# Kernel optimization log

Hardware: AMD Instinct MI355X
Metric: run time of the kernel (lower is better)

## Reference

```python
import jax, jax.numpy as jnp
import numpy as np

NUM_WIRES = 4
N_LAYERS = 2
HIDDEN = 64
NUM_CLASSES = 10
B = 4096


def _ry(state, theta, wire):
    # state: (N,2,2,2,2); theta: scalar or (N,)
    st = jnp.moveaxis(state, wire + 1, 1)
    c = jnp.reshape(jnp.cos(theta / 2), (-1, 1, 1, 1))
    s = jnp.reshape(jnp.sin(theta / 2), (-1, 1, 1, 1))
    n0 = c * st[:, 0] - s * st[:, 1]
    n1 = s * st[:, 0] + c * st[:, 1]
    st = jnp.stack([n0, n1], axis=1)
    return jnp.moveaxis(st, 1, wire + 1)


def _cnot(state, ctrl, tgt):
    st = jnp.moveaxis(state, (ctrl + 1, tgt + 1), (1, 2))  # (N,2,2,2,2)
    st = jnp.stack([st[:, 0], st[:, 1, ::-1]], axis=1)
    return jnp.moveaxis(st, (1, 2), (ctrl + 1, tgt + 1))


def _zexp(state, wire):
    p = state * state  # real statevector -> probabilities
    axes = tuple(a for a in range(1, 5) if a != wire + 1)
    marg = p.sum(axes)  # (N,2)
    return marg[:, 0] - marg[:, 1]


def quantum_layer(angles, vparams):
    # angles: (N,4) data rotation angles; vparams: (2,4)
    N = angles.shape[0]
    state = jnp.zeros((N, 2, 2, 2, 2), angles.dtype).at[:, 0, 0, 0, 0].set(1.0)
    for w in range(NUM_WIRES):
        state = _ry(state, angles[:, w], w)
    for l in range(N_LAYERS):
        for w in range(NUM_WIRES):
            state = _ry(state, vparams[l, w], w)
        state = _cnot(state, 0, 1)
        state = _cnot(state, 1, 2)
        state = _cnot(state, 2, 3)
    return jnp.stack([_zexp(state, w) for w in range(NUM_WIRES)], axis=1)  # (N,4)


def setup_inputs() -> dict:
    key = jax.random.key(0)
    ks = jax.random.split(key, 8)
    x = jax.random.uniform(ks[0], (B, 28, 28), dtype=jnp.float32)
    vparams = jax.random.normal(ks[1], (N_LAYERS, NUM_WIRES), dtype=jnp.float32)
    w1 = jax.random.normal(ks[2], (HIDDEN, NUM_WIRES), dtype=jnp.float32) * 0.5
    b1 = jnp.zeros((HIDDEN,), jnp.float32)
    w2 = jax.random.normal(ks[3], (1, HIDDEN), dtype=jnp.float32) * 0.125
    b2 = jnp.zeros((1,), jnp.float32)
    W = jax.random.normal(ks[4], (NUM_CLASSES, NUM_WIRES * 14 * 14), dtype=jnp.float32) * 0.03
    b = jnp.zeros((NUM_CLASSES,), jnp.float32)
    return {"x": x, "vparams": vparams, "w1": w1, "b1": b1, "w2": w2, "b2": b2, "W": W, "b": b}


def reference(x, vparams, w1, b1, w2, b2, W, b):
    Bx = x.shape[0]
    # 2x2 stride-2 patches, order [(r,c),(r,c+1),(r+1,c),(r+1,c+1)], patches row-major
    patches = x.reshape(Bx, 14, 2, 14, 2).transpose(0, 1, 3, 2, 4).reshape(Bx, 196, 4)
    meas = quantum_layer(patches.reshape(-1, 4), vparams).reshape(Bx, 196, 4)
    h = jax.nn.relu(jnp.einsum('bpn,hn->bph', meas, w1) + b1)
    scores = (jnp.einsum('bph,oh->bpo', h, w2) + b2)[..., 0]  # (B,196)
    attn = jax.nn.softmax(scores, axis=1)[..., None]
    weighted = meas * attn
    flat = weighted.reshape(Bx, -1)  # (B,784)
    logits = flat @ W.T + b
    return jax.nn.log_softmax(logits, axis=-1)
```

## Files before the change

kernel.cpp:

```cpp
#include <hip/hip_runtime.h>
#include <math.h>

#define NP 196
#define NC 10

template<int CTRL>
__device__ __forceinline__ float dpp_sum_step(float x) {
    int t = __builtin_amdgcn_update_dpp(0, __float_as_int(x), CTRL, 0xf, 0xf, false);
    return x + __int_as_float(t);
}
template<int CTRL>
__device__ __forceinline__ float dpp_max_step(float x) {
    int xi = __float_as_int(x);
    int t = __builtin_amdgcn_update_dpp(xi, xi, CTRL, 0xf, 0xf, false);
    return fmaxf(x, __int_as_float(t));
}
__device__ __forceinline__ float wave_sum(float x) {
    x = dpp_sum_step<0x111>(x);
    x = dpp_sum_step<0x112>(x);
    x = dpp_sum_step<0x114>(x);
    x = dpp_sum_step<0x118>(x);
    x = dpp_sum_step<0x142>(x);
    x = dpp_sum_step<0x143>(x);
    return __int_as_float(__builtin_amdgcn_readlane(__float_as_int(x), 63));
}
__device__ __forceinline__ float wave_max(float x) {
    x = dpp_max_step<0x111>(x);
    x = dpp_max_step<0x112>(x);
    x = dpp_max_step<0x114>(x);
    x = dpp_max_step<0x118>(x);
    x = dpp_max_step<0x142>(x);
    x = dpp_max_step<0x143>(x);
    return __int_as_float(__builtin_amdgcn_readlane(__float_as_int(x), 63));
}

__global__ __launch_bounds__(256) void quanv_fused(
    const float* __restrict__ x,
    const float* __restrict__ vparams,
    const float* __restrict__ w1,
    const float* __restrict__ b1,
    const float* __restrict__ w2,
    const float* __restrict__ b2,
    const float* __restrict__ W,
    const float* __restrict__ bias,
    float* __restrict__ out)
{
    __shared__ float s_red_max[4];
    __shared__ float s_red_sum[4];
    __shared__ float s_lred[4][NC];
    __shared__ float s_logits[NC];

    const int tid  = threadIdx.x;
    const int b    = blockIdx.x;
    const int lane = tid & 63;
    const int wv   = tid >> 6;

    float meas0 = 0.f, meas1 = 0.f, meas2 = 0.f, meas3 = 0.f;
    float myscore = -INFINITY;
    if (tid < NP) {
        const int pr = tid / 14;
        const int pc = tid - pr * 14;
        const float* px = x + (size_t)b * 784 + (2 * pr) * 28 + 2 * pc;
        const float2 ra = *(const float2*)px;
        const float2 rb = *(const float2*)(px + 28);

        float cw[4], sw[4];
        __sincosf((ra.x + vparams[0]) * 0.5f, &sw[0], &cw[0]);
        __sincosf((ra.y + vparams[1]) * 0.5f, &sw[1], &cw[1]);
        __sincosf((rb.x + vparams[2]) * 0.5f, &sw[2], &cw[2]);
        __sincosf((rb.y + vparams[3]) * 0.5f, &sw[3], &cw[3]);

        float t[4] = {cw[0]*cw[1], cw[0]*sw[1], sw[0]*cw[1], sw[0]*sw[1]};
        float u[4] = {cw[2]*cw[3], cw[2]*sw[3], sw[2]*cw[3], sw[2]*sw[3]};
        float v[16];
        #pragma unroll
        for (int i = 0; i < 16; i++) v[i] = t[i >> 2] * u[i & 3];

        #pragma unroll
        for (int i = 0; i < 16; i++)
            if ((i & 8) && !(i & 4)) { const float tm = v[i]; v[i] = v[i | 4]; v[i | 4] = tm; }
        #pragma unroll
        for (int i = 0; i < 16; i++)
            if ((i & 4) && !(i & 2)) { const float tm = v[i]; v[i] = v[i | 2]; v[i | 2] = tm; }
        #pragma unroll
        for (int i = 0; i < 16; i++)
            if ((i & 2) && !(i & 1)) { const float tm = v[i]; v[i] = v[i | 1]; v[i | 1] = tm; }

        #pragma unroll
        for (int w = 0; w < 4; w++) {
            float c, s;
            __sincosf(vparams[4 + w] * 0.5f, &s, &c);
            const int m = 8 >> w;
            #pragma unroll
            for (int i = 0; i < 16; i++) {
                if ((i & m) == 0) {
                    const float v0 = v[i], v1 = v[i | m];
                    v[i]     = c * v0 - s * v1;
                    v[i | m] = s * v0 + c * v1;
                }
            }
        }
        #pragma unroll
        for (int i = 0; i < 16; i++)
            if ((i & 8) && !(i & 4)) { const float tm = v[i]; v[i] = v[i | 4]; v[i | 4] = tm; }
        #pragma unroll
        for (int i = 0; i < 16; i++)
            if ((i & 4) && !(i & 2)) { const float tm = v[i]; v[i] = v[i | 2]; v[i | 2] = tm; }
        #pragma unroll
        for (int i = 0; i < 16; i++)
            if ((i & 2) && !(i & 1)) { const float tm = v[i]; v[i] = v[i | 1]; v[i | 1] = tm; }

        float p[16];
        #pragma unroll
        for (int i = 0; i < 16; i++) p[i] = v[i] * v[i];
        float e[8], d[8];
        #pragma unroll
        for (int j = 0; j < 8; j++) { e[j] = p[2*j] + p[2*j+1]; d[j] = p[2*j] - p[2*j+1]; }
        meas3 = ((d[0]+d[1]) + (d[2]+d[3])) + ((d[4]+d[5]) + (d[6]+d[7]));
        float f[4], g[4];
        #pragma unroll
        for (int k = 0; k < 4; k++) { f[k] = e[2*k] + e[2*k+1]; g[k] = e[2*k] - e[2*k+1]; }
        meas2 = (g[0]+g[1]) + (g[2]+g[3]);
        meas1 = (f[0]-f[1]) + (f[2]-f[3]);
        meas0 = (f[0]+f[1]) - (f[2]+f[3]);

        float sc = b2[0];
        #pragma unroll
        for (int j = 0; j < 64; j++) {
            float h = fmaf(w1[j * 4 + 0], meas0, fmaf(w1[j * 4 + 1], meas1,
                      fmaf(w1[j * 4 + 2], meas2, fmaf(w1[j * 4 + 3], meas3, b1[j]))));
            h = fmaxf(h, 0.f);
            sc = fmaf(w2[j], h, sc);
        }
        myscore = sc;
    }

    float mx = wave_max(myscore);
    if (lane == 0) s_red_max[wv] = mx;
    __syncthreads();
    const float gmax = fmaxf(fmaxf(s_red_max[0], s_red_max[1]),
                             fmaxf(s_red_max[2], s_red_max[3]));
    const float e2 = (tid < NP) ? __expf(myscore - gmax) : 0.f;
    float sm = wave_sum(e2);
    if (lane == 0) s_red_sum[wv] = sm;
    __syncthreads();
    const float gsum = s_red_sum[0] + s_red_sum[1] + s_red_sum[2] + s_red_sum[3];
    const float attn = e2 / gsum;

    float acc[NC];
    #pragma unroll
    for (int o = 0; o < NC; o++) acc[o] = 0.f;
    if (tid < NP) {
        const float wm0 = attn * meas0, wm1 = attn * meas1;
        const float wm2 = attn * meas2, wm3 = attn * meas3;
        #pragma unroll
        for (int o = 0; o < NC; o++) {
            const float4 Wv = *(const float4*)(W + o * 784 + tid * 4);
            acc[o] = fmaf(wm0, Wv.x, fmaf(wm1, Wv.y, fmaf(wm2, Wv.z, wm3 * Wv.w)));
        }
    }
    #pragma unroll
    for (int o = 0; o < NC; o++) {
        const float a = wave_sum(acc[o]);
        if (lane == 0) s_lred[wv][o] = a;
    }
    __syncthreads();
    if (tid < NC) {
        s_logits[tid] = bias[tid] + s_lred[0][tid] + s_lred[1][tid]
                      + s_lred[2][tid] + s_lred[3][tid];
    }
    __syncthreads();
    if (tid < NC) {
        float lmax = s_logits[0];
        #pragma unroll
        for (int i = 1; i < NC; i++) lmax = fmaxf(lmax, s_logits[i]);
        float lse = 0.f;
        #pragma unroll
        for (int i = 0; i < NC; i++) lse += __expf(s_logits[i] - lmax);
        out[(size_t)b * NC + tid] = s_logits[tid] - lmax - __logf(lse);
    }
}

extern "C" void kernel_launch(void* const* d_in, const int* in_sizes, int n_in,
                              void* d_out, int out_size, void* d_ws, size_t ws_size,
                              hipStream_t stream) {
    const float* x       = (const float*)d_in[0];
    const float* vparams = (const float*)d_in[1];
    const float* w1      = (const float*)d_in[2];
    const float* b1      = (const float*)d_in[3];
    const float* w2      = (const float*)d_in[4];
    const float* b2      = (const float*)d_in[5];
    const float* W       = (const float*)d_in[6];
    const float* bias    = (const float*)d_in[7];
    float* out           = (float*)d_out;

    const int B = in_sizes[0] / 784;
    quanv_fused<<<B, 256, 0, stream>>>(x, vparams, w1, b1, w2, b2, W, bias, out);
}
```

Before: 94.83 us.

## Drop softmax max pass and merge normalizer into single reduction round

Removes the max-subtraction pass of the attention softmax, computing exp(score) directly and folding the normalizing sum into the same reduction as the ten logit partial sums. Reductions now use 16-lane DPP row sums written to shared memory and summed by 11 threads, cutting a block barrier and the cross-row DPP steps. Out-of-range threads are clamped to a valid patch so the per-patch math runs without branching, and the hidden-layer loop uses two accumulators. Skipping the max subtraction risks overflow or precision loss if scores become large.

Result: faster. 90.13 us (-5.0%).

```diff
diff --git a/kernel.cpp b/kernel.cpp
--- a/kernel.cpp
+++ b/kernel.cpp
@@ -9,29 +9,12 @@
     int t = __builtin_amdgcn_update_dpp(0, __float_as_int(x), CTRL, 0xf, 0xf, false);
     return x + __int_as_float(t);
 }
-template<int CTRL>
-__device__ __forceinline__ float dpp_max_step(float x) {
-    int xi = __float_as_int(x);
-    int t = __builtin_amdgcn_update_dpp(xi, xi, CTRL, 0xf, 0xf, false);
-    return fmaxf(x, __int_as_float(t));
-}
-__device__ __forceinline__ float wave_sum(float x) {
+__device__ __forceinline__ float row16_sum(float x) {
     x = dpp_sum_step<0x111>(x);
     x = dpp_sum_step<0x112>(x);
     x = dpp_sum_step<0x114>(x);
     x = dpp_sum_step<0x118>(x);
-    x = dpp_sum_step<0x142>(x);
-    x = dpp_sum_step<0x143>(x);
-    return __int_as_float(__builtin_amdgcn_readlane(__float_as_int(x), 63));
-}
-__device__ __forceinline__ float wave_max(float x) {
-    x = dpp_max_step<0x111>(x);
-    x = dpp_max_step<0x112>(x);
-    x = dpp_max_step<0x114>(x);
-    x = dpp_max_step<0x118>(x);
-    x = dpp_max_step<0x142>(x);
-    x = dpp_max_step<0x143>(x);
-    return __int_as_float(__builtin_amdgcn_readlane(__float_as_int(x), 63));
+    return x;
 }
 
 __global__ __launch_bounds__(256) void quanv_fused(
@@ -45,131 +28,128 @@
     const float* __restrict__ bias,
     float* __restrict__ out)
 {
-    __shared__ float s_red_max[4];
-    __shared__ float s_red_sum[4];
-    __shared__ float s_lred[4][NC];
+    __shared__ float s_part[11][16];
+    __shared__ float s_tot[11];
     __shared__ float s_logits[NC];
 
     const int tid  = threadIdx.x;
     const int b    = blockIdx.x;
     const int lane = tid & 63;
     const int wv   = tid >> 6;
+    const int pt   = (tid < NP) ? tid : NP - 1;
 
-    float meas0 = 0.f, meas1 = 0.f, meas2 = 0.f, meas3 = 0.f;
-    float myscore = -INFINITY;
-    if (tid < NP) {
-        const int pr = tid / 14;
-        const int pc = tid - pr * 14;
-        const float* px = x + (size_t)b * 784 + (2 * pr) * 28 + 2 * pc;
-        const float2 ra = *(const float2*)px;
-        const float2 rb = *(const float2*)(px + 28);
+    const int pr = pt / 14;
+    const int pc = pt - pr * 14;
+    const float* px = x + (size_t)b * 784 + (2 * pr) * 28 + 2 * pc;
+    const float2 ra = *(const float2*)px;
+    const float2 rb = *(const float2*)(px + 28);
 
-        float cw[4], sw[4];
-        __sincosf((ra.x + vparams[0]) * 0.5f, &sw[0], &cw[0]);
-        __sincosf((ra.y + vparams[1]) * 0.5f, &sw[1], &cw[1]);
-        __sincosf((rb.x + vparams[2]) * 0.5f, &sw[2], &cw[2]);
-        __sincosf((rb.y + vparams[3]) * 0.5f, &sw[3], &cw[3]);
+    float cw[4], sw[4];
+    __sincosf((ra.x + vparams[0]) * 0.5f, &sw[0], &cw[0]);
+    __sincosf((ra.y + vparams[1]) * 0.5f, &sw[1], &cw[1]);
+    __sincosf((rb.x + vparams[2]) * 0.5f, &sw[2], &cw[2]);
+    __sincosf((rb.y + vparams[3]) * 0.5f, &sw[3], &cw[3]);
 
-        float t[4] = {cw[0]*cw[1], cw[0]*sw[1], sw[0]*cw[1], sw[0]*sw[1]};
-        float u[4] = {cw[2]*cw[3], cw[2]*sw[3], sw[2]*cw[3], sw[2]*sw[3]};
-        float v[16];
+    float t[4] = {cw[0]*cw[1], cw[0]*sw[1], sw[0]*cw[1], sw[0]*sw[1]};
+    float u[4] = {cw[2]*cw[3], cw[2]*sw[3], sw[2]*cw[3], sw[2]*sw[3]};
+    float v[16];
+    #pragma unroll
+    for (int i = 0; i < 16; i++) v[i] = t[i >> 2] * u[i & 3];
+
+    #pragma unroll
+    for (int i = 0; i < 16; i++)
+        if ((i & 8) && !(i & 4)) { const float tm = v[i]; v[i] = v[i | 4]; v[i | 4] = tm; }
+    #pragma unroll
+    for (int i = 0; i < 16; i++)
+        if ((i & 4) && !(i & 2)) { const float tm = v[i]; v[i] = v[i | 2]; v[i | 2] = tm; }
+    #pragma unroll
+    for (int i = 0; i < 16; i++)
+        if ((i & 2) && !(i & 1)) { const float tm = v[i]; v[i] = v[i | 1]; v[i | 1] = tm; }
+
+    #pragma unroll
+    for (int w = 0; w < 4; w++) {
+        float c, s;
+        __sincosf(vparams[4 + w] * 0.5f, &s, &c);
+        const int m = 8 >> w;
         #pragma unroll
-        for (int i = 0; i < 16; i++) v[i] = t[i >> 2] * u[i & 3];
-
-        #pragma unroll
-        for (int i = 0; i < 16; i++)
-            if ((i & 8) && !(i & 4)) { const float tm = v[i]; v[i] = v[i | 4]; v[i | 4] = tm; }
-        #pragma unroll
-        for (int i = 0; i < 16; i++)
-            if ((i & 4) && !(i & 2)) { const float tm = v[i]; v[i] = v[i | 2]; v[i | 2] = tm; }
-        #pragma unroll
-        for (int i = 0; i < 16; i++)
-            if ((i & 2) && !(i & 1)) { const float tm = v[i]; v[i] = v[i | 1]; v[i | 1] = tm; }
-
-        #pragma unroll
-        for (int w = 0; w < 4; w++) {
-            float c, s;
-            __sincosf(vparams[4 + w] * 0.5f, &s, &c);
-            const int m = 8 >> w;
-            #pragma unroll
-            for (int i = 0; i < 16; i++) {
-                if ((i & m) == 0) {
-                    const float v0 = v[i], v1 = v[i | m];
-                    v[i]     = c * v0 - s * v1;
-                    v[i | m] = s * v0 + c * v1;
-                }
+        for (int i = 0; i < 16; i++) {
+            if ((i & m) == 0) {
+                const float v0 = v[i], v1 = v[i | m];
+                v[i]     = c * v0 - s * v1;
+                v[i | m] = s * v0 + c * v1;
             }
-        }
-        #pragma unroll
-        for (int i = 0; i < 16; i++)
-            if ((i & 8) && !(i & 4)) { const float tm = v[i]; v[i] = v[i | 4]; v[i | 4] = tm; }
-        #pragma unroll
-        for (int i = 0; i < 16; i++)
-            if ((i & 4) && !(i & 2)) { const float tm = v[i]; v[i] = v[i | 2]; v[i | 2] = tm; }
-        #pragma unroll
-        for (int i = 0; i < 16; i++)
-            if ((i & 2) && !(i & 1)) { const float tm = v[i]; v[i] = v[i | 1]; v[i | 1] = tm; }
-
-        float p[16];
-        #pragma unroll
-        for (int i = 0; i < 16; i++) p[i] = v[i] * v[i];
-        float e[8], d[8];
-        #pragma unroll
-        for (int j = 0; j < 8; j++) { e[j] = p[2*j] + p[2*j+1]; d[j] = p[2*j] - p[2*j+1]; }
-        meas3 = ((d[0]+d[1]) + (d[2]+d[3])) + ((d[4]+d[5]) + (d[6]+d[7]));
-        float f[4], g[4];
-        #pragma unroll
-        for (int k = 0; k < 4; k++) { f[k] = e[2*k] + e[2*k+1]; g[k] = e[2*k] - e[2*k+1]; }
-        meas2 = (g[0]+g[1]) + (g[2]+g[3]);
-        meas1 = (f[0]-f[1]) + (f[2]-f[3]);
-        meas0 = (f[0]+f[1]) - (f[2]+f[3]);
-
-        float sc = b2[0];
-        #pragma unroll
-        for (int j = 0; j < 64; j++) {
-            float h = fmaf(w1[j * 4 + 0], meas0, fmaf(w1[j * 4 + 1], meas1,
-                      fmaf(w1[j * 4 + 2], meas2, fmaf(w1[j * 4 + 3], meas3, b1[j]))));
-            h = fmaxf(h, 0.f);
-            sc = fmaf(w2[j], h, sc);
-        }
-        myscore = sc;
-    }
-
-    float mx = wave_max(myscore);
-    if (lane == 0) s_red_max[wv] = mx;
-    __syncthreads();
-    const float gmax = fmaxf(fmaxf(s_red_max[0], s_red_max[1]),
-                             fmaxf(s_red_max[2], s_red_max[3]));
-    const float e2 = (tid < NP) ? __expf(myscore - gmax) : 0.f;
-    float sm = wave_sum(e2);
-    if (lane == 0) s_red_sum[wv] = sm;
-    __syncthreads();
-    const float gsum = s_red_sum[0] + s_red_sum[1] + s_red_sum[2] + s_red_sum[3];
-    const float attn = e2 / gsum;
-
-    float acc[NC];
-    #pragma unroll
-    for (int o = 0; o < NC; o++) acc[o] = 0.f;
-    if (tid < NP) {
-        const float wm0 = attn * meas0, wm1 = attn * meas1;
-        const float wm2 = attn * meas2, wm3 = attn * meas3;
-        #pragma unroll
-        for (int o = 0; o < NC; o++) {
-            const float4 Wv = *(const float4*)(W + o * 784 + tid * 4);
-            acc[o] = fmaf(wm0, Wv.x, fmaf(wm1, Wv.y, fmaf(wm2, Wv.z, wm3 * Wv.w)));
         }
     }
     #pragma unroll
+    for (int i = 0; i < 16; i++)
+        if ((i & 8) && !(i & 4)) { const float tm = v[i]; v[i] = v[i | 4]; v[i | 4] = tm; }
+    #pragma unroll
+    for (int i = 0; i < 16; i++)
+        if ((i & 4) && !(i & 2)) { const float tm = v[i]; v[i] = v[i | 2]; v[i | 2] = tm; }
+    #pragma unroll
+    for (int i = 0; i < 16; i++)
+        if ((i & 2) && !(i & 1)) { const float tm = v[i]; v[i] = v[i | 1]; v[i | 1] = tm; }
+
+    float p[16];
+    #pragma unroll
+    for (int i = 0; i < 16; i++) p[i] = v[i] * v[i];
+    float e8[8], d8[8];
+    #pragma unroll
+    for (int j = 0; j < 8; j++) { e8[j] = p[2*j] + p[2*j+1]; d8[j] = p[2*j] - p[2*j+1]; }
+    const float meas3 = ((d8[0]+d8[1]) + (d8[2]+d8[3])) + ((d8[4]+d8[5]) + (d8[6]+d8[7]));
+    float f4[4], g4[4];
+    #pragma unroll
+    for (int k = 0; k < 4; k++) { f4[k] = e8[2*k] + e8[2*k+1]; g4[k] = e8[2*k] - e8[2*k+1]; }
+    const float meas2 = (g4[0]+g4[1]) + (g4[2]+g4[3]);
+    const float meas1 = (f4[0]-f4[1]) + (f4[2]-f4[3]);
+    const float meas0 = (f4[0]+f4[1]) - (f4[2]+f4[3]);
+
+    float sca = b2[0], scb = 0.f;
+    #pragma unroll
+    for (int j = 0; j < 64; j += 2) {
+        float h0 = fmaf(w1[j*4 + 0], meas0, fmaf(w1[j*4 + 1], meas1,
+                   fmaf(w1[j*4 + 2], meas2, fmaf(w1[j*4 + 3], meas3, b1[j]))));
+        float h1 = fmaf(w1[j*4 + 4], meas0, fmaf(w1[j*4 + 5], meas1,
+                   fmaf(w1[j*4 + 6], meas2, fmaf(w1[j*4 + 7], meas3, b1[j+1]))));
+        sca = fmaf(w2[j],     fmaxf(h0, 0.f), sca);
+        scb = fmaf(w2[j + 1], fmaxf(h1, 0.f), scb);
+    }
+    const float sc = sca + scb;
+
+    const float e = (tid < NP) ? __expf(sc) : 0.f;
+    const float wm0 = e * meas0, wm1 = e * meas1;
+    const float wm2 = e * meas2, wm3 = e * meas3;
+
+    float r[11];
+    #pragma unroll
     for (int o = 0; o < NC; o++) {
-        const float a = wave_sum(acc[o]);
-        if (lane == 0) s_lred[wv][o] = a;
+        const float4 Wv = *(const float4*)(W + o * 784 + pt * 4);
+        r[o] = fmaf(wm0, Wv.x, fmaf(wm1, Wv.y, fmaf(wm2, Wv.z, wm3 * Wv.w)));
+    }
+    r[10] = e;
+
+    #pragma unroll
+    for (int i = 0; i < 11; i++) r[i] = row16_sum(r[i]);
+    if ((lane & 15) == 15) {
+        const int row = (wv << 2) | (lane >> 4);
+        #pragma unroll
+        for (int i = 0; i < 11; i++) s_part[i][row] = r[i];
     }
     __syncthreads();
-    if (tid < NC) {
-        s_logits[tid] = bias[tid] + s_lred[0][tid] + s_lred[1][tid]
-                      + s_lred[2][tid] + s_lred[3][tid];
+
+    if (tid < 11) {
+        const float4* q = (const float4*)s_part[tid];
+        const float4 a = q[0], c = q[1], d = q[2], g = q[3];
+        s_tot[tid] = (((a.x+a.y) + (a.z+a.w)) + ((c.x+c.y) + (c.z+c.w)))
+                   + (((d.x+d.y) + (d.z+d.w)) + ((g.x+g.y) + (g.z+g.w)));
     }
     __syncthreads();
+
+    if (tid < NC) {
+        s_logits[tid] = fmaf(s_tot[tid], __builtin_amdgcn_rcpf(s_tot[10]), bias[tid]);
+    }
+    __syncthreads();
+
     if (tid < NC) {
         float lmax = s_logits[0];
         #pragma unroll
```
